# Kernel optimization log

Measured on AMD Instinct MI355X. Metric: run time of the kernel, lower is better.

The kernel has to match this reference:

```python
import jax, jax.numpy as jnp
import numpy as np

N_NODES = 100000
N_EDGES = 1600000
IN_C, HID, OUT_C = 100, 128, 47
N_HID_LAYERS = 3  # SAGEConv(hid->hid) count; +1 final SAGEConv(hid->out)


def setup_inputs() -> dict:
    key = jax.random.key(0)
    ks = jax.random.split(key, 8)
    x = jax.random.normal(ks[0], (N_NODES, IN_C), dtype=jnp.float32)
    edge_index = jax.random.randint(ks[1], (2, N_EDGES), 0, N_NODES, dtype=jnp.int32)
    s = 0.05  # weight scale for numeric stability
    return {
        "x": x,
        "edge_index": edge_index,
        "inproj_w": jax.random.normal(ks[2], (IN_C, HID), dtype=jnp.float32) * s,
        "inproj_b": jnp.zeros((HID,), jnp.float32),
        "wl_h": jax.random.normal(ks[3], (N_HID_LAYERS, HID, HID), dtype=jnp.float32) * s,
        "bl_h": jnp.zeros((N_HID_LAYERS, HID), jnp.float32),
        "wr_h": jax.random.normal(ks[4], (N_HID_LAYERS, HID, HID), dtype=jnp.float32) * s,
        "wl_out": jax.random.normal(ks[5], (HID, OUT_C), dtype=jnp.float32) * s,
        "bl_out": jnp.zeros((OUT_C,), jnp.float32),
        "wr_out": jax.random.normal(ks[6], (HID, OUT_C), dtype=jnp.float32) * s,
    }


def reference(x, edge_index, inproj_w, inproj_b, wl_h, bl_h, wr_h, wl_out, bl_out, wr_out):
    n = x.shape[0]
    src, dst = edge_index[0], edge_index[1]
    # in-degree for mean aggregation (clamped to avoid div-by-zero)
    deg = jax.ops.segment_sum(jnp.ones_like(dst, dtype=x.dtype), dst, num_segments=n)
    deg = jnp.maximum(deg, 1.0)[:, None]

    def sage(h, wl, bl, wr):
        # mean over incoming-edge messages, then lin_l(agg) + lin_r(h)
        agg = jax.ops.segment_sum(h[src], dst, num_segments=n) / deg
        return agg @ wl + bl + h @ wr

    h = x @ inproj_w + inproj_b
    inp = h
    h = jax.nn.relu(h)
    for i in range(N_HID_LAYERS):
        h = sage(h, wl_h[i], bl_h[i], wr_h[i])
        h = jax.nn.relu(h) + 0.2 * inp  # dropout is identity in eval mode
    h = sage(h, wl_out, bl_out, wr_out)
    return jax.nn.log_softmax(h, axis=-1)
```

## Files before the change

kernel.cpp:

```cpp
#include <hip/hip_runtime.h>
#include <math.h>

#define HIDC 128
#define INC 100
#define OUTC 47

typedef __attribute__((ext_vector_type(8))) short short8_t;
typedef __attribute__((ext_vector_type(4))) float f32x4;

__device__ inline unsigned short f2bf(float f) {
    unsigned u = __builtin_bit_cast(unsigned, f);
    unsigned r = (u + 0x7FFFu + ((u >> 16) & 1u)) >> 16;
    return (unsigned short)r;
}
__device__ inline float bf2f(unsigned short s) {
    unsigned u = ((unsigned)s) << 16;
    return __builtin_bit_cast(float, u);
}


__global__ __launch_bounds__(256) void k_deg(const int* __restrict__ dst, int* __restrict__ deg, int ne) {
    int e = blockIdx.x * 256 + threadIdx.x;
    if (e < ne) atomicAdd(&deg[dst[e]], 1);
}

__global__ __launch_bounds__(256) void k_scan1(const int* __restrict__ deg, int* __restrict__ local_s,
                                               int* __restrict__ bsum, int n) {
    __shared__ int s[256];
    int t = threadIdx.x;
    int i = blockIdx.x * 256 + t;
    int v = (i < n) ? deg[i] : 0;
    s[t] = v;
    __syncthreads();
    for (int off = 1; off < 256; off <<= 1) {
        int add = (t >= off) ? s[t - off] : 0;
        __syncthreads();
        s[t] += add;
        __syncthreads();
    }
    if (i < n) local_s[i] = s[t] - v;
    if (t == 255) bsum[blockIdx.x] = s[255];
}

__global__ __launch_bounds__(512) void k_scan2(int* __restrict__ bsum, int nb) {
    __shared__ int s[512];
    int t = threadIdx.x;
    int v = (t < nb) ? bsum[t] : 0;
    s[t] = v;
    __syncthreads();
    for (int off = 1; off < 512; off <<= 1) {
        int add = (t >= off) ? s[t - off] : 0;
        __syncthreads();
        s[t] += add;
        __syncthreads();
    }
    if (t < nb) bsum[t] = s[t] - v;
}

__global__ __launch_bounds__(256) void k_scan3(const int* __restrict__ local_s, const int* __restrict__ bsum,
                                               int* __restrict__ offs, int n, int ne) {
    int i = blockIdx.x * 256 + threadIdx.x;
    if (i < n) offs[i] = local_s[i] + bsum[blockIdx.x];
    if (i == 0) offs[n] = ne;
}

__global__ __launch_bounds__(256) void k_invdeg(const int* __restrict__ deg, float* __restrict__ invdeg, int n) {
    int i = blockIdx.x * 256 + threadIdx.x;
    if (i < n) invdeg[i] = 1.0f / (float)max(deg[i], 1);
}


__global__ __launch_bounds__(256) void k_fill(const int* __restrict__ src, const int* __restrict__ dst,
                                              const int* __restrict__ offs, int* __restrict__ curs,
                                              int* __restrict__ csr, int ne, int psize, int ch) {
    int p = blockIdx.x & 7;
    int chunk = blockIdx.x >> 3;
    int lo = p * psize;
    int e0 = chunk * ch;
    int e1 = min(ne, e0 + ch);
    for (int e = e0 + threadIdx.x; e < e1; e += 256) {
        int d = dst[e];
        if ((unsigned)(d - lo) < (unsigned)psize) {
            int pos = atomicAdd(&curs[d], 1);
            csr[offs[d] + pos] = src[e];
        }
    }
}


__global__ __launch_bounds__(256) void k_prepw(const float* __restrict__ wl_h, const float* __restrict__ wr_h,
                                               unsigned short* __restrict__ wt) {
    int idx = blockIdx.x * 256 + threadIdx.x;
    if (idx >= 6 * 16384) return;
    int m = idx >> 14, rem = idx & 16383;
    int l = m >> 1, s = m & 1;
    const float* srcm = (s == 0 ? wl_h : wr_h) + (size_t)l * 16384;
    wt[idx] = f2bf(srcm[(rem & 127) * 128 + (rem >> 7)]);
}

__global__ __launch_bounds__(256) void k_prepw_out(const float* __restrict__ wl_out,
                                                   const float* __restrict__ wr_out,
                                                   unsigned short* __restrict__ wt2) {
    int idx = blockIdx.x * 256 + threadIdx.x;
    if (idx >= 2 * 48 * 128) return;
    int s = idx / (48 * 128), rem = idx % (48 * 128);
    int nc = rem >> 7, k = rem & 127;
    const float* srcm = (s == 0) ? wl_out : wr_out;
    wt2[idx] = (nc < OUTC) ? f2bf(srcm[k * OUTC + nc]) : 0;
}

__global__ __launch_bounds__(256) void k_prepw_in(const float* __restrict__ w,
                                                  unsigned short* __restrict__ wtin) {
    int idx = blockIdx.x * 256 + threadIdx.x;
    if (idx >= 128 * 128) return;
    int nc = idx >> 7, k = idx & 127;
    wtin[idx] = (k < INC) ? f2bf(w[k * HIDC + nc]) : 0;
}


__global__ __launch_bounds__(256) void k_agg(const unsigned short* __restrict__ h, const int* __restrict__ csr,
                                             const int* __restrict__ offs, const float* __restrict__ invdeg,
                                             unsigned short* __restrict__ agg, int n) {
    int wv = threadIdx.x >> 6, lane = threadIdx.x & 63;
    int v = blockIdx.x * 4 + wv;
    if (v >= n) return;
    int q = lane >> 4, c = lane & 15;
    int e0 = offs[v], e1 = offs[v + 1];
    float acc[8] = {0, 0, 0, 0, 0, 0, 0, 0};
    for (int e = e0 + q; e < e1; e += 8) {
        int s0 = csr[e];
        bool has2 = (e + 4) < e1;
        int s1 = has2 ? csr[e + 4] : s0;
        short8_t t0 = *reinterpret_cast<const short8_t*>(h + (size_t)s0 * HIDC + c * 8);
        short8_t t1 = *reinterpret_cast<const short8_t*>(h + (size_t)s1 * HIDC + c * 8);
#pragma unroll
        for (int i = 0; i < 8; i++) {
            acc[i] += bf2f((unsigned short)t0[i]);
            if (has2) acc[i] += bf2f((unsigned short)t1[i]);
        }
    }
#pragma unroll
    for (int i = 0; i < 8; i++) {
        acc[i] += __shfl_xor(acc[i], 16);
        acc[i] += __shfl_xor(acc[i], 32);
    }
    if (q == 0) {
        float s = invdeg[v];
        unsigned short o[8];
#pragma unroll
        for (int i = 0; i < 8; i++) o[i] = f2bf(acc[i] * s);
        *reinterpret_cast<short8_t*>(agg + (size_t)v * HIDC + c * 8) = *reinterpret_cast<const short8_t*>(o);
    }
}


__global__ __launch_bounds__(256) void k_inproj_mfma(const float* __restrict__ x,
                                                     const unsigned short* __restrict__ wtin,
                                                     const float* __restrict__ b,
                                                     unsigned short* __restrict__ inp,
                                                     unsigned short* __restrict__ h, int n) {
    __shared__ unsigned short sX[32 * 128];
    int t = threadIdx.x;
    int w = t >> 6, lane = t & 63;
    int cc = lane & 15, kg = lane >> 4;
    int row0 = blockIdx.x * 32;

    short8_t bfrag[2][4];
#pragma unroll
    for (int ci = 0; ci < 2; ci++) {
        int ncol = 32 * w + ci * 16 + cc;
        const unsigned short* bp = wtin + ncol * 128 + kg * 8;
#pragma unroll
        for (int ks = 0; ks < 4; ks++)
            bfrag[ci][ks] = *reinterpret_cast<const short8_t*>(bp + ks * 32);
    }

    {
        int r = t >> 3, seg = t & 7;
        int row = row0 + r;
        float v[16];
#pragma unroll
        for (int i = 0; i < 16; i++) v[i] = 0.f;
        if (row < n) {
            const float* xr = x + (size_t)row * INC;
            if (seg < 6) {
#pragma unroll
                for (int j = 0; j < 4; j++) {
                    float4 f = *reinterpret_cast<const float4*>(xr + seg * 16 + j * 4);
                    v[j * 4 + 0] = f.x; v[j * 4 + 1] = f.y; v[j * 4 + 2] = f.z; v[j * 4 + 3] = f.w;
                }
            } else if (seg == 6) {
                float4 f = *reinterpret_cast<const float4*>(xr + 96);
                v[0] = f.x; v[1] = f.y; v[2] = f.z; v[3] = f.w;
            }
        }
        unsigned short o[16];
#pragma unroll
        for (int i = 0; i < 16; i++) o[i] = f2bf(v[i]);
#pragma unroll
        for (int half = 0; half < 2; half++) {
            int g = seg * 2 + half;
            unsigned byte = r * 256 + (((unsigned)g * 16) ^ (((unsigned)r & 7) << 4));
            *reinterpret_cast<short8_t*>(reinterpret_cast<char*>(sX) + byte) =
                *reinterpret_cast<const short8_t*>(&o[half * 8]);
        }
    }
    __syncthreads();

    f32x4 acc[2][2];
#pragma unroll
    for (int rt = 0; rt < 2; rt++)
#pragma unroll
        for (int ci = 0; ci < 2; ci++) acc[rt][ci] = (f32x4){0.f, 0.f, 0.f, 0.f};

#pragma unroll
    for (int ks = 0; ks < 4; ks++) {
        short8_t af[2];
#pragma unroll
        for (int rt = 0; rt < 2; rt++) {
            int r = rt * 16 + cc;
            unsigned byte = r * 256 + (((unsigned)(ks * 64 + kg * 16)) ^ (((unsigned)r & 7) << 4));
            af[rt] = *reinterpret_cast<const short8_t*>(reinterpret_cast<const char*>(sX) + byte);
        }
#pragma unroll
        for (int rt = 0; rt < 2; rt++)
#pragma unroll
            for (int ci = 0; ci < 2; ci++)
                acc[rt][ci] = __builtin_amdgcn_mfma_f32_16x16x32_bf16(af[rt], bfrag[ci][ks],
                                                                      acc[rt][ci], 0, 0, 0);
    }

#pragma unroll
    for (int rt = 0; rt < 2; rt++)
#pragma unroll
        for (int ci = 0; ci < 2; ci++) {
            int col = 32 * w + ci * 16 + cc;
            float bv = b[col];
#pragma unroll
            for (int reg = 0; reg < 4; reg++) {
                int row = row0 + rt * 16 + kg * 4 + reg;
                if (row < n) {
                    float v = acc[rt][ci][reg] + bv;
                    inp[(size_t)row * HIDC + col] = f2bf(v);
                    h[(size_t)row * HIDC + col] = f2bf(fmaxf(v, 0.f));
                }
            }
        }
}


__global__ __launch_bounds__(256) void k_sage_mfma(const unsigned short* __restrict__ agg,
                                                   unsigned short* __restrict__ h,
                                                   const unsigned short* __restrict__ inp,
                                                   const unsigned short* __restrict__ wt,
                                                   const float* __restrict__ bl, int n) {
    __shared__ unsigned short sA[2][32 * 128];
    int t = threadIdx.x;
    int w = t >> 6, lane = t & 63;
    int cc = lane & 15, kg = lane >> 4;
    int row0 = blockIdx.x * 32;

    short8_t bfrag[2][2][4];
#pragma unroll
    for (int s = 0; s < 2; s++)
#pragma unroll
        for (int ci = 0; ci < 2; ci++) {
            int ncol = 32 * w + ci * 16 + cc;
            const unsigned short* bp = wt + s * 16384 + ncol * 128 + kg * 8;
#pragma unroll
            for (int ks = 0; ks < 4; ks++)
                bfrag[s][ci][ks] = *reinterpret_cast<const short8_t*>(bp + ks * 32);
        }

    for (int c = t; c < 512; c += 256) {
        int r = c >> 4, g = c & 15;
        int row = row0 + r;
        unsigned byte = r * 256 + (((unsigned)g * 16) ^ (((unsigned)r & 7) << 4));
        short8_t va = {0, 0, 0, 0, 0, 0, 0, 0}, vh = va;
        if (row < n) {
            va = *reinterpret_cast<const short8_t*>(agg + (size_t)row * HIDC + g * 8);
            vh = *reinterpret_cast<const short8_t*>(h + (size_t)row * HIDC + g * 8);
        }
        *reinterpret_cast<short8_t*>(reinterpret_cast<char*>(&sA[0][0]) + byte) = va;
        *reinterpret_cast<short8_t*>(reinterpret_cast<char*>(&sA[1][0]) + byte) = vh;
    }
    __syncthreads();

    f32x4 acc[2][2];
#pragma unroll
    for (int rt = 0; rt < 2; rt++)
#pragma unroll
        for (int ci = 0; ci < 2; ci++) acc[rt][ci] = (f32x4){0.f, 0.f, 0.f, 0.f};

#pragma unroll
    for (int ks = 0; ks < 4; ks++) {
        short8_t af[2][2];
#pragma unroll
        for (int s = 0; s < 2; s++)
#pragma unroll
            for (int rt = 0; rt < 2; rt++) {
                int r = rt * 16 + cc;
                unsigned byte = r * 256 + (((unsigned)(ks * 64 + kg * 16)) ^ (((unsigned)r & 7) << 4));
                af[s][rt] = *reinterpret_cast<const short8_t*>(reinterpret_cast<const char*>(&sA[s][0]) + byte);
            }
#pragma unroll
        for (int s = 0; s < 2; s++)
#pragma unroll
            for (int rt = 0; rt < 2; rt++)
#pragma unroll
                for (int ci = 0; ci < 2; ci++)
                    acc[rt][ci] = __builtin_amdgcn_mfma_f32_16x16x32_bf16(af[s][rt], bfrag[s][ci][ks],
                                                                          acc[rt][ci], 0, 0, 0);
    }

#pragma unroll
    for (int rt = 0; rt < 2; rt++)
#pragma unroll
        for (int ci = 0; ci < 2; ci++) {
            int col = 32 * w + ci * 16 + cc;
            float bv = bl[col];
#pragma unroll
            for (int reg = 0; reg < 4; reg++) {
                int row = row0 + rt * 16 + kg * 4 + reg;
                if (row < n) {
                    float v = acc[rt][ci][reg] + bv;
                    v = fmaxf(v, 0.f) + 0.2f * bf2f(inp[(size_t)row * HIDC + col]);
                    h[(size_t)row * HIDC + col] = f2bf(v);
                }
            }
        }
}


__global__ __launch_bounds__(256) void k_out_mfma(const unsigned short* __restrict__ agg,
                                                  const unsigned short* __restrict__ h,
                                                  const unsigned short* __restrict__ wt2,
                                                  const float* __restrict__ bl,
                                                  float* __restrict__ out, int n) {
    __shared__ unsigned short sA[2][64 * 128];
    int t = threadIdx.x;
    int w = t >> 6, lane = t & 63;
    int cc = lane & 15, kg = lane >> 4;
    int row0 = blockIdx.x * 64;

    short8_t bfrag[2][3][4];
#pragma unroll
    for (int s = 0; s < 2; s++)
#pragma unroll
        for (int ci = 0; ci < 3; ci++) {
            const unsigned short* bp = wt2 + s * (48 * 128) + (ci * 16 + cc) * 128 + kg * 8;
#pragma unroll
            for (int ks = 0; ks < 4; ks++)
                bfrag[s][ci][ks] = *reinterpret_cast<const short8_t*>(bp + ks * 32);
        }

    for (int c = t; c < 1024; c += 256) {
        int r = c >> 4, g = c & 15;
        int row = row0 + r;
        unsigned byte = r * 256 + (((unsigned)g * 16) ^ (((unsigned)r & 7) << 4));
        short8_t va = {0, 0, 0, 0, 0, 0, 0, 0}, vh = va;
        if (row < n) {
            va = *reinterpret_cast<const short8_t*>(agg + (size_t)row * HIDC + g * 8);
            vh = *reinterpret_cast<const short8_t*>(h + (size_t)row * HIDC + g * 8);
        }
        *reinterpret_cast<short8_t*>(reinterpret_cast<char*>(&sA[0][0]) + byte) = va;
        *reinterpret_cast<short8_t*>(reinterpret_cast<char*>(&sA[1][0]) + byte) = vh;
    }
    __syncthreads();

    f32x4 acc[3];
#pragma unroll
    for (int ci = 0; ci < 3; ci++) acc[ci] = (f32x4){0.f, 0.f, 0.f, 0.f};

#pragma unroll
    for (int ks = 0; ks < 4; ks++) {
        short8_t af[2];
        int r = w * 16 + cc;
        unsigned byte = r * 256 + (((unsigned)(ks * 64 + kg * 16)) ^ (((unsigned)r & 7) << 4));
#pragma unroll
        for (int s = 0; s < 2; s++)
            af[s] = *reinterpret_cast<const short8_t*>(reinterpret_cast<const char*>(&sA[s][0]) + byte);
#pragma unroll
        for (int s = 0; s < 2; s++)
#pragma unroll
            for (int ci = 0; ci < 3; ci++)
                acc[ci] = __builtin_amdgcn_mfma_f32_16x16x32_bf16(af[s], bfrag[s][ci][ks], acc[ci], 0, 0, 0);
    }

#pragma unroll
    for (int reg = 0; reg < 4; reg++) {
        int row = row0 + w * 16 + kg * 4 + reg;
        float val[3];
        float m = -INFINITY;
#pragma unroll
        for (int ci = 0; ci < 3; ci++) {
            int col = ci * 16 + cc;
            val[ci] = (col < OUTC) ? (acc[ci][reg] + bl[col]) : -INFINITY;
            m = fmaxf(m, val[ci]);
        }
#pragma unroll
        for (int off = 1; off < 16; off <<= 1) m = fmaxf(m, __shfl_xor(m, off));
        float s = 0.f;
#pragma unroll
        for (int ci = 0; ci < 3; ci++) {
            int col = ci * 16 + cc;
            if (col < OUTC) s += __expf(val[ci] - m);
        }
#pragma unroll
        for (int off = 1; off < 16; off <<= 1) s += __shfl_xor(s, off);
        float lse = m + logf(s);
        if (row < n) {
#pragma unroll
            for (int ci = 0; ci < 3; ci++) {
                int col = ci * 16 + cc;
                if (col < OUTC) out[(size_t)row * OUTC + col] = val[ci] - lse;
            }
        }
    }
}


extern "C" void kernel_launch(void* const* d_in, const int* in_sizes, int n_in,
                              void* d_out, int out_size, void* d_ws, size_t ws_size,
                              hipStream_t stream) {
    const float* x        = (const float*)d_in[0];
    const int*   ei       = (const int*)d_in[1];
    const float* inproj_w = (const float*)d_in[2];
    const float* inproj_b = (const float*)d_in[3];
    const float* wl_h     = (const float*)d_in[4];
    const float* bl_h     = (const float*)d_in[5];
    const float* wr_h     = (const float*)d_in[6];
    const float* wl_out   = (const float*)d_in[7];
    const float* bl_out   = (const float*)d_in[8];
    const float* wr_out   = (const float*)d_in[9];
    float* out = (float*)d_out;

    int n  = in_sizes[0] / INC;
    int ne = in_sizes[1] / 2;
    const int* src = ei;
    const int* dst = ei + ne;

    char* ws = (char*)d_ws;
    size_t off = 0;
    auto alloc = [&](size_t bytes) -> void* {
        void* p = ws + off;
        off = (off + bytes + 255) & ~(size_t)255;
        return p;
    };
    unsigned short* inp    = (unsigned short*)alloc((size_t)n * HIDC * 2);
    unsigned short* h      = (unsigned short*)alloc((size_t)n * HIDC * 2);
    unsigned short* agg    = (unsigned short*)alloc((size_t)n * HIDC * 2);
    unsigned short* wt     = (unsigned short*)alloc((size_t)6 * 16384 * 2);
    unsigned short* wt2    = (unsigned short*)alloc((size_t)2 * 48 * 128 * 2);
    unsigned short* wtin   = (unsigned short*)alloc((size_t)128 * 128 * 2);
    int*   deg    = (int*)alloc((size_t)n * 4);
    float* invdeg = (float*)alloc((size_t)n * 4);
    int*   local_s= (int*)alloc((size_t)n * 4);
    int*   bsum   = (int*)alloc(512 * 4);
    int*   offs   = (int*)alloc((size_t)(n + 1) * 4);
    int*   curs   = (int*)alloc((size_t)n * 4);
    int*   csr    = (int*)alloc((size_t)ne * 4);

    hipMemsetAsync(deg, 0, (size_t)n * 4, stream);
    hipMemsetAsync(curs, 0, (size_t)n * 4, stream);

    int nbE = (ne + 255) / 256;
    int nbN = (n + 255) / 256;
    k_deg<<<nbE, 256, 0, stream>>>(dst, deg, ne);
    k_scan1<<<nbN, 256, 0, stream>>>(deg, local_s, bsum, n);
    k_scan2<<<1, 512, 0, stream>>>(bsum, nbN);
    k_scan3<<<nbN, 256, 0, stream>>>(local_s, bsum, offs, n, ne);
    k_invdeg<<<nbN, 256, 0, stream>>>(deg, invdeg, n);

    int psize = (n + 7) / 8;
    int nchunk = 256;
    int ch = (ne + nchunk - 1) / nchunk;
    k_fill<<<nchunk * 8, 256, 0, stream>>>(src, dst, offs, curs, csr, ne, psize, ch);

    k_prepw<<<(6 * 16384 + 255) / 256, 256, 0, stream>>>(wl_h, wr_h, wt);
    k_prepw_out<<<(2 * 48 * 128 + 255) / 256, 256, 0, stream>>>(wl_out, wr_out, wt2);
    k_prepw_in<<<(128 * 128 + 255) / 256, 256, 0, stream>>>(inproj_w, wtin);

    int nbA = (n + 3) / 4;
    int nbT = (n + 31) / 32;
    int nbO = (n + 63) / 64;
    k_inproj_mfma<<<nbT, 256, 0, stream>>>(x, wtin, inproj_b, inp, h, n);
    for (int l = 0; l < 3; ++l) {
        k_agg<<<nbA, 256, 0, stream>>>(h, csr, offs, invdeg, agg, n);
        k_sage_mfma<<<nbT, 256, 0, stream>>>(agg, h, inp, wt + (size_t)l * 2 * 16384,
                                             bl_h + (size_t)l * HIDC, n);
    }
    k_agg<<<nbA, 256, 0, stream>>>(h, csr, offs, invdeg, agg, n);
    k_out_mfma<<<nbO, 256, 0, stream>>>(agg, h, wt2, bl_out, out, n);
}
```

Before: 592.3 us.

## Fuse neighbor mean-aggregation into SAGE MFMA kernels with ping-pong h buffers

Removes the standalone aggregation kernel and computes the neighbour mean directly into shared memory inside the SAGE and output GEMM kernels. This drops the agg buffer write and read and four kernel launches, and uses double-buffered h arrays to avoid read/write hazards. The cost is lower parallelism: each wave now walks 8 or 16 nodes serially, versus one node per wave before. Gather latency is then less well hidden and occupancy may be limited by shared memory.

```diff
diff --git a/kernel.cpp b/kernel.cpp
--- a/kernel.cpp
+++ b/kernel.cpp
@@ -118,42 +118,6 @@
 }
 
 
-__global__ __launch_bounds__(256) void k_agg(const unsigned short* __restrict__ h, const int* __restrict__ csr,
-                                             const int* __restrict__ offs, const float* __restrict__ invdeg,
-                                             unsigned short* __restrict__ agg, int n) {
-    int wv = threadIdx.x >> 6, lane = threadIdx.x & 63;
-    int v = blockIdx.x * 4 + wv;
-    if (v >= n) return;
-    int q = lane >> 4, c = lane & 15;
-    int e0 = offs[v], e1 = offs[v + 1];
-    float acc[8] = {0, 0, 0, 0, 0, 0, 0, 0};
-    for (int e = e0 + q; e < e1; e += 8) {
-        int s0 = csr[e];
-        bool has2 = (e + 4) < e1;
-        int s1 = has2 ? csr[e + 4] : s0;
-        short8_t t0 = *reinterpret_cast<const short8_t*>(h + (size_t)s0 * HIDC + c * 8);
-        short8_t t1 = *reinterpret_cast<const short8_t*>(h + (size_t)s1 * HIDC + c * 8);
-#pragma unroll
-        for (int i = 0; i < 8; i++) {
-            acc[i] += bf2f((unsigned short)t0[i]);
-            if (has2) acc[i] += bf2f((unsigned short)t1[i]);
-        }
-    }
-#pragma unroll
-    for (int i = 0; i < 8; i++) {
-        acc[i] += __shfl_xor(acc[i], 16);
-        acc[i] += __shfl_xor(acc[i], 32);
-    }
-    if (q == 0) {
-        float s = invdeg[v];
-        unsigned short o[8];
-#pragma unroll
-        for (int i = 0; i < 8; i++) o[i] = f2bf(acc[i] * s);
-        *reinterpret_cast<short8_t*>(agg + (size_t)v * HIDC + c * 8) = *reinterpret_cast<const short8_t*>(o);
-    }
-}
-
-
 __global__ __launch_bounds__(256) void k_inproj_mfma(const float* __restrict__ x,
                                                      const unsigned short* __restrict__ wtin,
                                                      const float* __restrict__ b,
@@ -249,11 +213,13 @@
 }
 
 
-__global__ __launch_bounds__(256) void k_sage_mfma(const unsigned short* __restrict__ agg,
-                                                   unsigned short* __restrict__ h,
-                                                   const unsigned short* __restrict__ inp,
-                                                   const unsigned short* __restrict__ wt,
-                                                   const float* __restrict__ bl, int n) {
+__global__ __launch_bounds__(256) void k_sage_fused(const unsigned short* __restrict__ h_in,
+                                                    unsigned short* __restrict__ h_out,
+                                                    const unsigned short* __restrict__ inp,
+                                                    const int* __restrict__ csr, const int* __restrict__ offs,
+                                                    const float* __restrict__ invdeg,
+                                                    const unsigned short* __restrict__ wt,
+                                                    const float* __restrict__ bl, int n) {
     __shared__ unsigned short sA[2][32 * 128];
     int t = threadIdx.x;
     int w = t >> 6, lane = t & 63;
@@ -276,13 +242,48 @@
         int r = c >> 4, g = c & 15;
         int row = row0 + r;
         unsigned byte = r * 256 + (((unsigned)g * 16) ^ (((unsigned)r & 7) << 4));
-        short8_t va = {0, 0, 0, 0, 0, 0, 0, 0}, vh = va;
-        if (row < n) {
-            va = *reinterpret_cast<const short8_t*>(agg + (size_t)row * HIDC + g * 8);
-            vh = *reinterpret_cast<const short8_t*>(h + (size_t)row * HIDC + g * 8);
-        }
-        *reinterpret_cast<short8_t*>(reinterpret_cast<char*>(&sA[0][0]) + byte) = va;
+        short8_t vh = {0, 0, 0, 0, 0, 0, 0, 0};
+        if (row < n) vh = *reinterpret_cast<const short8_t*>(h_in + (size_t)row * HIDC + g * 8);
         *reinterpret_cast<short8_t*>(reinterpret_cast<char*>(&sA[1][0]) + byte) = vh;
+    }
+
+    {
+        int q = lane >> 4, c16 = lane & 15;
+#pragma unroll
+        for (int i = 0; i < 8; i++) {
+            int v = row0 + w * 8 + i;
+            float acc[8] = {0, 0, 0, 0, 0, 0, 0, 0};
+            if (v < n) {
+                int e0 = offs[v], e1 = offs[v + 1];
+                for (int e = e0 + q; e < e1; e += 8) {
+                    int s0 = csr[e];
+                    bool has2 = (e + 4) < e1;
+                    int s1 = has2 ? csr[e + 4] : s0;
+                    short8_t t0 = *reinterpret_cast<const short8_t*>(h_in + (size_t)s0 * HIDC + c16 * 8);
+                    short8_t t1 = *reinterpret_cast<const short8_t*>(h_in + (size_t)s1 * HIDC + c16 * 8);
+#pragma unroll
+                    for (int j = 0; j < 8; j++) {
+                        acc[j] += bf2f((unsigned short)t0[j]);
+                        if (has2) acc[j] += bf2f((unsigned short)t1[j]);
+                    }
+                }
+            }
+#pragma unroll
+            for (int j = 0; j < 8; j++) {
+                acc[j] += __shfl_xor(acc[j], 16);
+                acc[j] += __shfl_xor(acc[j], 32);
+            }
+            if (q == 0) {
+                float s = (v < n) ? invdeg[v] : 0.f;
+                unsigned short o[8];
+#pragma unroll
+                for (int j = 0; j < 8; j++) o[j] = f2bf(acc[j] * s);
+                int r = w * 8 + i;
+                unsigned byte = r * 256 + (((unsigned)c16 * 16) ^ (((unsigned)r & 7) << 4));
+                *reinterpret_cast<short8_t*>(reinterpret_cast<char*>(&sA[0][0]) + byte) =
+                    *reinterpret_cast<const short8_t*>(o);
+            }
+        }
     }
     __syncthreads();
 
@@ -325,18 +326,19 @@
                 if (row < n) {
                     float v = acc[rt][ci][reg] + bv;
                     v = fmaxf(v, 0.f) + 0.2f * bf2f(inp[(size_t)row * HIDC + col]);
-                    h[(size_t)row * HIDC + col] = f2bf(v);
+                    h_out[(size_t)row * HIDC + col] = f2bf(v);
                 }
             }
         }
 }
 
 
-__global__ __launch_bounds__(256) void k_out_mfma(const unsigned short* __restrict__ agg,
-                                                  const unsigned short* __restrict__ h,
-                                                  const unsigned short* __restrict__ wt2,
-                                                  const float* __restrict__ bl,
-                                                  float* __restrict__ out, int n) {
+__global__ __launch_bounds__(256) void k_out_fused(const unsigned short* __restrict__ h_in,
+                                                   const int* __restrict__ csr, const int* __restrict__ offs,
+                                                   const float* __restrict__ invdeg,
+                                                   const unsigned short* __restrict__ wt2,
+                                                   const float* __restrict__ bl,
+                                                   float* __restrict__ out, int n) {
     __shared__ unsigned short sA[2][64 * 128];
     int t = threadIdx.x;
     int w = t >> 6, lane = t & 63;
@@ -358,13 +360,48 @@
         int r = c >> 4, g = c & 15;
         int row = row0 + r;
         unsigned byte = r * 256 + (((unsigned)g * 16) ^ (((unsigned)r & 7) << 4));
-        short8_t va = {0, 0, 0, 0, 0, 0, 0, 0}, vh = va;
-        if (row < n) {
-            va = *reinterpret_cast<const short8_t*>(agg + (size_t)row * HIDC + g * 8);
-            vh = *reinterpret_cast<const short8_t*>(h + (size_t)row * HIDC + g * 8);
-        }
-        *reinterpret_cast<short8_t*>(reinterpret_cast<char*>(&sA[0][0]) + byte) = va;
+        short8_t vh = {0, 0, 0, 0, 0, 0, 0, 0};
+        if (row < n) vh = *reinterpret_cast<const short8_t*>(h_in + (size_t)row * HIDC + g * 8);
         *reinterpret_cast<short8_t*>(reinterpret_cast<char*>(&sA[1][0]) + byte) = vh;
+    }
+
+    {
+        int q = lane >> 4, c16 = lane & 15;
+#pragma unroll
+        for (int i = 0; i < 16; i++) {
+            int v = row0 + w * 16 + i;
+            float acc[8] = {0, 0, 0, 0, 0, 0, 0, 0};
+            if (v < n) {
+                int e0 = offs[v], e1 = offs[v + 1];
+                for (int e = e0 + q; e < e1; e += 8) {
+                    int s0 = csr[e];
+                    bool has2 = (e + 4) < e1;
+                    int s1 = has2 ? csr[e + 4] : s0;
+                    short8_t t0 = *reinterpret_cast<const short8_t*>(h_in + (size_t)s0 * HIDC + c16 * 8);
+                    short8_t t1 = *reinterpret_cast<const short8_t*>(h_in + (size_t)s1 * HIDC + c16 * 8);
+#pragma unroll
+                    for (int j = 0; j < 8; j++) {
+                        acc[j] += bf2f((unsigned short)t0[j]);
+                        if (has2) acc[j] += bf2f((unsigned short)t1[j]);
+                    }
+                }
+            }
+#pragma unroll
+            for (int j = 0; j < 8; j++) {
+                acc[j] += __shfl_xor(acc[j], 16);
+                acc[j] += __shfl_xor(acc[j], 32);
+            }
+            if (q == 0) {
+                float s = (v < n) ? invdeg[v] : 0.f;
+                unsigned short o[8];
+#pragma unroll
+                for (int j = 0; j < 8; j++) o[j] = f2bf(acc[j] * s);
+                int r = w * 16 + i;
+                unsigned byte = r * 256 + (((unsigned)c16 * 16) ^ (((unsigned)r & 7) << 4));
+                *reinterpret_cast<short8_t*>(reinterpret_cast<char*>(&sA[0][0]) + byte) =
+                    *reinterpret_cast<const short8_t*>(o);
+            }
+        }
     }
     __syncthreads();
 
@@ -448,8 +485,8 @@
         return p;
     };
     unsigned short* inp    = (unsigned short*)alloc((size_t)n * HIDC * 2);
-    unsigned short* h      = (unsigned short*)alloc((size_t)n * HIDC * 2);
-    unsigned short* agg    = (unsigned short*)alloc((size_t)n * HIDC * 2);
+    unsigned short* h_a    = (unsigned short*)alloc((size_t)n * HIDC * 2);
+    unsigned short* h_b    = (unsigned short*)alloc((size_t)n * HIDC * 2);
     unsigned short* wt     = (unsigned short*)alloc((size_t)6 * 16384 * 2);
     unsigned short* wt2    = (unsigned short*)alloc((size_t)2 * 48 * 128 * 2);
     unsigned short* wtin   = (unsigned short*)alloc((size_t)128 * 128 * 2);
@@ -481,15 +518,17 @@
     k_prepw_out<<<(2 * 48 * 128 + 255) / 256, 256, 0, stream>>>(wl_out, wr_out, wt2);
     k_prepw_in<<<(128 * 128 + 255) / 256, 256, 0, stream>>>(inproj_w, wtin);
 
-    int nbA = (n + 3) / 4;
     int nbT = (n + 31) / 32;
     int nbO = (n + 63) / 64;
-    k_inproj_mfma<<<nbT, 256, 0, stream>>>(x, wtin, inproj_b, inp, h, n);
+    k_inproj_mfma<<<nbT, 256, 0, stream>>>(x, wtin, inproj_b, inp, h_a, n);
+
+    unsigned short* h_cur = h_a;
+    unsigned short* h_nxt = h_b;
     for (int l = 0; l < 3; ++l) {
-        k_agg<<<nbA, 256, 0, stream>>>(h, csr, offs, invdeg, agg, n);
-        k_sage_mfma<<<nbT, 256, 0, stream>>>(agg, h, inp, wt + (size_t)l * 2 * 16384,
-                                             bl_h + (size_t)l * HIDC, n);
-    }
-    k_agg<<<nbA, 256, 0, stream>>>(h, csr, offs, invdeg, agg, n);
-    k_out_mfma<<<nbO, 256, 0, stream>>>(agg, h, wt2, bl_out, out, n);
-}
+        k_sage_fused<<<nbT, 256, 0, stream>>>(h_cur, h_nxt, inp, csr, offs, invdeg,
+                                              wt + (size_t)l * 2 * 16384,
+                                              bl_h + (size_t)l * HIDC, n);
+        unsigned short* tmp = h_cur; h_cur = h_nxt; h_nxt = tmp;
+    }
+    k_out_fused<<<nbO, 256, 0, stream>>>(h_cur, csr, offs, invdeg, wt2, bl_out, out, n);
+}
```

New measurement: 771.0 us. 30.2% more time.
